# Kernel optimization log

Hardware: AMD Instinct MI355X
Metric: run time of the kernel (lower is better)

The kernel has to match this reference:

```python
import jax, jax.numpy as jnp
import numpy as np
import math

B, S, D = 2, 1024, 512
H = 8
DH = D // H
N_NEURONS = 512
K = 16
N_BASIS = 8
RANK = 64
D_FF = 2048
LN_EPS = 1e-5


def _layer_norm(x, g, b):
    mu = jnp.mean(x, axis=-1, keepdims=True)
    var = jnp.var(x, axis=-1, keepdims=True)
    return (x - mu) * jax.lax.rsqrt(var + LN_EPS) * g + b


def setup_inputs() -> dict:
    key = jax.random.key(0)
    ks = jax.random.split(key, 16)
    x = jax.random.normal(ks[0], (B, S, D), dtype=jnp.float32)
    # causal mask [B,1,S,S] (True = keep)
    mask = jnp.broadcast_to(jnp.tril(jnp.ones((S, S), dtype=bool)), (B, 1, S, S))
    inp = {
        "x": x,
        "neuron_emb": jax.random.normal(ks[1], (N_NEURONS, D)) * 0.02,
        "Wq": jax.random.normal(ks[2], (D, D)) * 0.02, "bq": jnp.zeros((D,)),
        "Wk": jax.random.normal(ks[3], (D, D)) * 0.02, "bk": jnp.zeros((D,)),
        "Wv": jax.random.normal(ks[4], (D, D)) * 0.02, "bv": jnp.zeros((D,)),
        "Wg": jax.random.normal(ks[5], (2 * D, 2)) * 0.02, "bg": jnp.zeros((2,)),
        "basis_A": jax.random.normal(ks[6], (N_BASIS, D, RANK)) * 0.05,
        "basis_B": jax.random.normal(ks[7], (N_BASIS, RANK, D_FF)) * 0.05,
        "neuron_coords": jax.random.normal(ks[8], (N_NEURONS, N_BASIS)) * 0.5,
        "Wd": jax.random.normal(ks[9], (D_FF, D)) * 0.02, "bd": jnp.zeros((D,)),
        "ln1_g": jnp.ones((D,)), "ln1_b": jnp.zeros((D,)),
        "ln2_g": jnp.ones((D,)), "ln2_b": jnp.zeros((D,)),
        "mask": mask,
    }
    return inp


def reference(x, neuron_emb, Wq, bq, Wk, bk, Wv, bv, Wg, bg, basis_A, basis_B,
              neuron_coords, Wd, bd, ln1_g, ln1_b, ln2_g, ln2_b, mask):
    normed = _layer_norm(x, ln1_g, ln1_b)
    # --- router: cross-attention context ---
    q = (normed @ Wq + bq).reshape(B, S, H, DH).transpose(0, 2, 1, 3)
    k = (normed @ Wk + bk).reshape(B, S, H, DH).transpose(0, 2, 1, 3)
    v = (normed @ Wv + bv).reshape(B, S, H, DH).transpose(0, 2, 1, 3)
    attn = jnp.einsum('bhsd,bhtd->bhst', q, k) / math.sqrt(DH)
    attn = jnp.where(mask, attn, -jnp.inf)
    attn = jax.nn.softmax(attn, axis=-1)
    context = jnp.einsum('bhst,bhtd->bhsd', attn, v)
    context = context.transpose(0, 2, 1, 3).reshape(B, S, D)
    # --- gated neuron scoring + top-k ---
    token_scores = normed @ neuron_emb.T            # [B,S,N]
    context_scores = context @ neuron_emb.T         # [B,S,N]
    gate = jax.nn.softmax(jnp.concatenate([normed, context], axis=-1) @ Wg + bg, axis=-1)
    scores = gate[:, :, 0:1] * token_scores + gate[:, :, 1:2] * context_scores
    topk_scores, topk_idx = jax.lax.top_k(scores, K)  # [B,S,K]
    weights = jax.nn.softmax(topk_scores, axis=-1)
    # --- neuron info residual ---
    neuron_info = jnp.einsum('bsk,bskd->bsd', weights, neuron_emb[topk_idx])
    x = x + neuron_info
    # --- per-token basis-mixed low-rank FFN ---
    normed2 = _layer_norm(x, ln2_g, ln2_b)
    coords = neuron_coords[topk_idx]                # [B,S,K,n_basis]
    token_coords = jnp.einsum('bsk,bskn->bsn', weights, coords)  # [B,S,n_basis]
    # h = x @ (sum_n c_n A_n): contract without materializing [B,S,D,R]
    h = jnp.einsum('bsnr,bsn->bsr', jnp.einsum('bsd,ndr->bsnr', normed2, basis_A), token_coords)
    h = jnp.einsum('bsnf,bsn->bsf', jnp.einsum('bsr,nrf->bsnf', h, basis_B), token_coords)
    h = jax.nn.gelu(h, approximate=False)
    out = h @ Wd + bd
    x = x + out
    return (x, topk_idx)
```

## Files before the change

kernel.cpp:

```cpp
#include <hip/hip_runtime.h>
#include <hip/hip_bf16.h>

#define Bv 2
#define Sv 1024
#define Dv 512
#define Hv 8
#define Nv 512
#define Kv 16
#define NBv 8
#define DFv 2048
#define NTOK (Bv*Sv)

typedef __attribute__((ext_vector_type(8))) short short8;
typedef __attribute__((ext_vector_type(4))) float float4v;

__launch_bounds__(256)
__global__ void ln64_k(const float* __restrict__ x, const float* __restrict__ g,
                       const float* __restrict__ b, double* __restrict__ out)
{
    const int t = blockIdx.x;
    const size_t base = (size_t)t * Dv;
    const int tid = threadIdx.x;
    double v0 = (double)x[base + tid];
    double v1 = (double)x[base + tid + 256];
    double s = v0 + v1, ss = v0 * v0 + v1 * v1;
    #pragma unroll
    for (int off = 32; off; off >>= 1) { s += __shfl_xor(s, off); ss += __shfl_xor(ss, off); }
    __shared__ double red[4][2];
    const int wv = tid >> 6, ln = tid & 63;
    if (ln == 0) { red[wv][0] = s; red[wv][1] = ss; }
    __syncthreads();
    s  = red[0][0] + red[1][0] + red[2][0] + red[3][0];
    ss = red[0][1] + red[1][1] + red[2][1] + red[3][1];
    double mu  = s * (1.0 / Dv);
    double var = ss * (1.0 / Dv) - mu * mu;
    double rstd = 1.0 / sqrt(var + 1e-5);
    out[base + tid]       = (v0 - mu) * rstd * (double)g[tid]       + (double)b[tid];
    out[base + tid + 256] = (v1 - mu) * rstd * (double)g[tid + 256] + (double)b[tid + 256];
}

__launch_bounds__(256)
__global__ void qkv64_k(const double* __restrict__ A,
                        const float* __restrict__ Wq, const float* __restrict__ Wk,
                        const float* __restrict__ Wv, const float* __restrict__ bq,
                        const float* __restrict__ bk, const float* __restrict__ bvv,
                        double* __restrict__ qo, double* __restrict__ ko,
                        double* __restrict__ vo)
{
    const int z = blockIdx.z;
    const float* Bm  = (z == 0) ? Wq : (z == 1) ? Wk : Wv;
    const float* bia = (z == 0) ? bq : (z == 1) ? bk : bvv;
    double* Cout     = (z == 0) ? qo : (z == 1) ? ko : vo;
    const int N = Dv, Kd = Dv;
    __shared__ double As[16][68];
    __shared__ double Bs[16][68];
    const int tid = threadIdx.x;
    const int m0 = blockIdx.y * 64, n0 = blockIdx.x * 64;
    const int tx = tid & 15, ty = tid >> 4;
    double acc[4][4] = {};
    const int lm = tid >> 2, lk4 = (tid & 3) << 2;
    for (int k0 = 0; k0 < Kd; k0 += 16) {
        double4 av = *(const double4*)(A + (size_t)(m0 + lm) * Kd + k0 + lk4);
        As[lk4 + 0][lm] = av.x; As[lk4 + 1][lm] = av.y;
        As[lk4 + 2][lm] = av.z; As[lk4 + 3][lm] = av.w;
        const int kk = tid >> 4, n4 = (tid & 15) << 2;
        float4 bv4 = *(const float4*)(Bm + (size_t)(k0 + kk) * N + n0 + n4);
        Bs[kk][n4 + 0] = (double)bv4.x; Bs[kk][n4 + 1] = (double)bv4.y;
        Bs[kk][n4 + 2] = (double)bv4.z; Bs[kk][n4 + 3] = (double)bv4.w;
        __syncthreads();
        #pragma unroll
        for (int kk2 = 0; kk2 < 16; kk2++) {
            double a_[4], b_[4];
            *(double4*)a_ = *(const double4*)&As[kk2][ty << 2];
            *(double4*)b_ = *(const double4*)&Bs[kk2][tx << 2];
            #pragma unroll
            for (int i = 0; i < 4; i++)
                #pragma unroll
                for (int j = 0; j < 4; j++)
                    acc[i][j] = fma(a_[i], b_[j], acc[i][j]);
        }
        __syncthreads();
    }
    #pragma unroll
    for (int i = 0; i < 4; i++) {
        const int row = m0 + (ty << 2) + i;
        #pragma unroll
        for (int j = 0; j < 4; j++) {
            const int col = n0 + (tx << 2) + j;
            Cout[(size_t)row * N + col] = acc[i][j] + (double)bia[col];
        }
    }
}

__launch_bounds__(256)
__global__ void scores64_k(const double* __restrict__ A0, const double* __restrict__ A1,
                           const double* __restrict__ gate, const float* __restrict__ Bm,
                           double* __restrict__ Cbase)
{
    const int M = NTOK, N = Nv, Kd = Dv;
    const int z = blockIdx.z;
    const int kbeg = z * (Dv / 2), kend = kbeg + Dv / 2;
    double* Cout = Cbase + (size_t)z * M * N;
    __shared__ double As[16][68];
    __shared__ double Bs[16][68];
    const int tid = threadIdx.x;
    const int m0 = blockIdx.y * 64, n0 = blockIdx.x * 64;
    const int tx = tid & 15, ty = tid >> 4;
    double acc[4][4] = {};
    const int lm = tid >> 2, lk4 = (tid & 3) << 2;
    for (int k0 = kbeg; k0 < kend; k0 += 16) {
        const double g0 = gate[2 * (m0 + lm)], g1 = gate[2 * (m0 + lm) + 1];
        double4 a0 = *(const double4*)(A0 + (size_t)(m0 + lm) * Kd + k0 + lk4);
        double4 a1 = *(const double4*)(A1 + (size_t)(m0 + lm) * Kd + k0 + lk4);
        As[lk4 + 0][lm] = g0 * a0.x + g1 * a1.x;
        As[lk4 + 1][lm] = g0 * a0.y + g1 * a1.y;
        As[lk4 + 2][lm] = g0 * a0.z + g1 * a1.z;
        As[lk4 + 3][lm] = g0 * a0.w + g1 * a1.w;
        const int nn = tid >> 2, kq = (tid & 3) << 2;
        float4 bv4 = *(const float4*)(Bm + (size_t)(n0 + nn) * Kd + k0 + kq);
        Bs[kq + 0][nn] = (double)bv4.x; Bs[kq + 1][nn] = (double)bv4.y;
        Bs[kq + 2][nn] = (double)bv4.z; Bs[kq + 3][nn] = (double)bv4.w;
        __syncthreads();
        #pragma unroll
        for (int kk = 0; kk < 16; kk++) {
            double a_[4], b_[4];
            *(double4*)a_ = *(const double4*)&As[kk][ty << 2];
            *(double4*)b_ = *(const double4*)&Bs[kk][tx << 2];
            #pragma unroll
            for (int i = 0; i < 4; i++)
                #pragma unroll
                for (int j = 0; j < 4; j++)
                    acc[i][j] = fma(a_[i], b_[j], acc[i][j]);
        }
        __syncthreads();
    }
    #pragma unroll
    for (int i = 0; i < 4; i++) {
        const int row = m0 + (ty << 2) + i;
        #pragma unroll
        for (int j = 0; j < 4; j++)
            Cout[(size_t)row * N + n0 + (tx << 2) + j] = acc[i][j];
    }
}

template<int EPI>
__launch_bounds__(256)
__global__ void mfma_k(const __hip_bfloat16* __restrict__ A, const __hip_bfloat16* __restrict__ B,
                       void* __restrict__ Cout_, int M, int N, int Kt, int kper)
{
    __shared__ __hip_bfloat16 As[128][40];
    __shared__ __hip_bfloat16 Bs[128][40];
    const int tid = threadIdx.x;
    const int m0 = blockIdx.y * 128, n0 = blockIdx.x * 128;
    const int z = blockIdx.z;
    const int kbeg = z * kper, kend = kbeg + kper;
    const int w = tid >> 6, l = tid & 63;
    const int wr = (w >> 1) * 64, wc = (w & 1) * 64;
    const int lm = l & 15, quad = l >> 4;
    float4v acc[4][4];
    #pragma unroll
    for (int i = 0; i < 4; i++)
        #pragma unroll
        for (int j = 0; j < 4; j++)
            acc[i][j] = (float4v){0.f, 0.f, 0.f, 0.f};
    const int srow = tid >> 1, skb = (tid & 1) * 16;
    for (int k0 = kbeg; k0 < kend; k0 += 32) {
        *(uint4*)&As[srow][skb]     = *(const uint4*)(A + (size_t)(m0 + srow) * Kt + k0 + skb);
        *(uint4*)&As[srow][skb + 8] = *(const uint4*)(A + (size_t)(m0 + srow) * Kt + k0 + skb + 8);
        *(uint4*)&Bs[srow][skb]     = *(const uint4*)(B + (size_t)(n0 + srow) * Kt + k0 + skb);
        *(uint4*)&Bs[srow][skb + 8] = *(const uint4*)(B + (size_t)(n0 + srow) * Kt + k0 + skb + 8);
        __syncthreads();
        short8 af[4], bf[4];
        #pragma unroll
        for (int mi = 0; mi < 4; mi++) af[mi] = *(const short8*)&As[wr + mi * 16 + lm][quad * 8];
        #pragma unroll
        for (int ni = 0; ni < 4; ni++) bf[ni] = *(const short8*)&Bs[wc + ni * 16 + lm][quad * 8];
        #pragma unroll
        for (int mi = 0; mi < 4; mi++)
            #pragma unroll
            for (int ni = 0; ni < 4; ni++)
                acc[mi][ni] = __builtin_amdgcn_mfma_f32_16x16x32_bf16(af[mi], bf[ni], acc[mi][ni], 0, 0, 0);
        __syncthreads();
    }
    #pragma unroll
    for (int mi = 0; mi < 4; mi++) {
        #pragma unroll
        for (int ni = 0; ni < 4; ni++) {
            const int col = n0 + wc + ni * 16 + lm;
            #pragma unroll
            for (int r = 0; r < 4; r++) {
                const int row = m0 + wr + mi * 16 + quad * 4 + r;
                float c = acc[mi][ni][r];
                if (EPI == 0) {
                    ((float*)Cout_)[(size_t)z * M * N + (size_t)row * N + col] = c;
                } else {
                    c = 0.5f * c * (1.0f + erff(c * 0.70710678118654752f));
                    ((__hip_bfloat16*)Cout_)[(size_t)row * N + col] = __float2bfloat16(c);
                }
            }
        }
    }
}

__device__ __constant__ int c_slotbase[4] = {0, 0, 384, 640};
__device__ __constant__ int c_cnt[4]      = {0, 24, 16, 8};

__launch_bounds__(256)
__global__ void attn64c_k(const double* __restrict__ q, const double* __restrict__ k,
                          const double* __restrict__ v, double* __restrict__ ctxun,
                          double* __restrict__ Opart, double* __restrict__ mbuf,
                          double* __restrict__ lbuf)
{
    const int qt = blockIdx.x, bh = blockIdx.y, ch = blockIdx.z;
    if (qt < ch * 8) return;
    const int b = bh >> 3, h = bh & 7;
    __shared__ double Qs[32][70];
    __shared__ double Kt[64][34];
    __shared__ double Vs[32][70];
    const int tid = threadIdx.x;
    const int r = tid >> 3, cc = tid & 7;
    const int lane = tid & 63;
    const int lbase = lane & 56;
    const size_t qoff = ((size_t)b * Sv + (size_t)qt * 32) * Dv + h * 64;
    #pragma unroll
    for (int i = 0; i < 4; i++) {
        int f = i * 256 + tid;
        int row = f >> 5, c2 = (f & 31) * 2;
        *(double2*)&Qs[row][c2] = *(const double2*)(q + qoff + (size_t)row * Dv + c2);
    }
    double O[8] = {};
    double mrun = -1e300, lrun = 0.0;
    const int iglob = qt * 32 + r;
    const int jbeg = ch * 8;
    const int jend = (qt < jbeg + 7) ? qt : (jbeg + 7);
    for (int jt = jbeg; jt <= jend; jt++) {
        __syncthreads();
        const size_t koff = ((size_t)b * Sv + (size_t)jt * 32) * Dv + h * 64;
        #pragma unroll
        for (int i = 0; i < 4; i++) {
            int f = i * 256 + tid;
            int row = f >> 5, c2 = (f & 31) * 2;
            double2 kv = *(const double2*)(k + koff + (size_t)row * Dv + c2);
            Kt[c2][row]     = kv.x;
            Kt[c2 + 1][row] = kv.y;
            *(double2*)&Vs[row][c2] = *(const double2*)(v + koff + (size_t)row * Dv + c2);
        }
        __syncthreads();
        double a[4] = {0.0, 0.0, 0.0, 0.0};
        #pragma unroll 8
        for (int kk = 0; kk < 64; kk += 2) {
            double2 qv  = *(const double2*)&Qs[r][kk];
            double2 ka0 = *(const double2*)&Kt[kk][cc * 4];
            double2 ka1 = *(const double2*)&Kt[kk][cc * 4 + 2];
            double2 kb0 = *(const double2*)&Kt[kk + 1][cc * 4];
            double2 kb1 = *(const double2*)&Kt[kk + 1][cc * 4 + 2];
            a[0] = fma(qv.x, ka0.x, fma(qv.y, kb0.x, a[0]));
            a[1] = fma(qv.x, ka0.y, fma(qv.y, kb0.y, a[1]));
            a[2] = fma(qv.x, ka1.x, fma(qv.y, kb1.x, a[2]));
            a[3] = fma(qv.x, ka1.y, fma(qv.y, kb1.y, a[3]));
        }
        double p[4];
        double mx = -1e300;
        #pragma unroll
        for (int jj = 0; jj < 4; jj++) {
            const int jglob = jt * 32 + cc * 4 + jj;
            p[jj] = (jglob <= iglob) ? a[jj] * 0.125 : -1e300;
            mx = fmax(mx, p[jj]);
        }
        mx = fmax(mx, __shfl_xor(mx, 1));
        mx = fmax(mx, __shfl_xor(mx, 2));
        mx = fmax(mx, __shfl_xor(mx, 4));
        const double mnew = fmax(mrun, mx);
        double rsum = 0.0;
        #pragma unroll
        for (int jj = 0; jj < 4; jj++) { p[jj] = exp(p[jj] - mnew); rsum += p[jj]; }
        rsum += __shfl_xor(rsum, 1);
        rsum += __shfl_xor(rsum, 2);
        rsum += __shfl_xor(rsum, 4);
        const double alpha = exp(mrun - mnew);
        lrun = lrun * alpha + rsum;
        mrun = mnew;
        #pragma unroll
        for (int c = 0; c < 8; c++) O[c] *= alpha;
        #pragma unroll
        for (int jsrc = 0; jsrc < 8; jsrc++) {
            #pragma unroll
            for (int jj = 0; jj < 4; jj++) {
                const double pj = __shfl(p[jj], lbase + jsrc);
                const double* vrow = &Vs[jsrc * 4 + jj][cc * 8];
                #pragma unroll
                for (int c2 = 0; c2 < 8; c2 += 2) {
                    double2 vv = *(const double2*)&vrow[c2];
                    O[c2 + 0] = fma(pj, vv.x, O[c2 + 0]);
                    O[c2 + 1] = fma(pj, vv.y, O[c2 + 1]);
                }
            }
        }
    }
    if (cc == 0) {
        const int mi = ((bh * 32 + qt) * 4 + ch) * 32 + r;
        mbuf[mi] = mrun; lbuf[mi] = lrun;
    }
    if (ch == 0) {
        const size_t obase = ((size_t)b * Sv + (size_t)iglob) * Dv + h * 64 + cc * 8;
        #pragma unroll
        for (int c2 = 0; c2 < 8; c2 += 2) { double2 t{O[c2], O[c2+1]}; *(double2*)(ctxun + obase + c2) = t; }
    } else {
        const int slot = c_slotbase[ch] + bh * c_cnt[ch] + (qt - ch * 8);
        const size_t obase = ((size_t)slot * 32 + r) * 64 + cc * 8;
        #pragma unroll
        for (int c2 = 0; c2 < 8; c2 += 2) { double2 t{O[c2], O[c2+1]}; *(double2*)(Opart + obase + c2) = t; }
    }
}

__launch_bounds__(256)
__global__ void attnmerge_k(double* __restrict__ ctx, const double* __restrict__ Opart,
                            const double* __restrict__ mbuf, const double* __restrict__ lbuf)
{
    const size_t i = (size_t)blockIdx.x * 256 + threadIdx.x;
    const size_t e = i * 2;
    const int d = (int)(e & 511);
    const int s = (int)((e >> 9) & 1023);
    const int b = (int)(e >> 19);
    const int h = d >> 6;
    const int qt = s >> 5, r = s & 31;
    const int bh = b * 8 + h;
    int nch = qt >> 3; if (nch > 3) nch = 3;
    const int mib = ((bh * 32 + qt) * 4) * 32 + r;
    double ms = mbuf[mib];
    for (int c = 1; c <= nch; c++) ms = fmax(ms, mbuf[mib + c * 32]);
    double2 o = *(const double2*)(ctx + e);
    double a0 = exp(mbuf[mib] - ms);
    double den = lbuf[mib] * a0;
    o.x *= a0; o.y *= a0;
    for (int c = 1; c <= nch; c++) {
        const double ac = exp(mbuf[mib + c * 32] - ms);
        den += lbuf[mib + c * 32] * ac;
        const int slot = c_slotbase[c] + bh * c_cnt[c] + (qt - c * 8);
        const size_t op = ((size_t)slot * 32 + r) * 64 + (d & 63);
        double2 oc = *(const double2*)(Opart + op);
        o.x = fma(ac, oc.x, o.x);
        o.y = fma(ac, oc.y, o.y);
    }
    const double inv = 1.0 / den;
    o.x *= inv; o.y *= inv;
    *(double2*)(ctx + e) = o;
}

__launch_bounds__(256)
__global__ void gate64_k(const double* __restrict__ normed, const double* __restrict__ ctx,
                         const float* __restrict__ Wg, const float* __restrict__ bg,
                         double* __restrict__ gate)
{
    const int wv = threadIdx.x >> 6, lane = threadIdx.x & 63;
    const int t = blockIdx.x * 4 + wv;
    double a0 = 0.0, a1 = 0.0;
    for (int d = lane; d < Dv; d += 64) {
        double nv = normed[(size_t)t * Dv + d];
        double cv = ctx[(size_t)t * Dv + d];
        a0 += nv * (double)Wg[2 * d]     + cv * (double)Wg[2 * (d + Dv)];
        a1 += nv * (double)Wg[2 * d + 1] + cv * (double)Wg[2 * (d + Dv) + 1];
    }
    #pragma unroll
    for (int off = 32; off; off >>= 1) { a0 += __shfl_xor(a0, off); a1 += __shfl_xor(a1, off); }
    if (lane == 0) {
        a0 += (double)bg[0]; a1 += (double)bg[1];
        double m = fmax(a0, a1);
        double e0 = exp(a0 - m), e1 = exp(a1 - m);
        double inv = 1.0 / (e0 + e1);
        gate[2 * t] = e0 * inv; gate[2 * t + 1] = e1 * inv;
    }
}

__launch_bounds__(256)
__global__ void topk64_k(const double* __restrict__ s0, const float* __restrict__ x,
                         const float* __restrict__ emb, const float* __restrict__ coords,
                         const float* __restrict__ g2, const float* __restrict__ b2,
                         float* __restrict__ x2, __hip_bfloat16* __restrict__ normed2bf,
                         float* __restrict__ tcoords, float* __restrict__ idx_out)
{
    __shared__ double sc[4][Nv];
    const int wv = threadIdx.x >> 6, lane = threadIdx.x & 63;
    const int t = blockIdx.x * 4 + wv;
    const double* s1 = s0 + (size_t)NTOK * Nv;
    double* s = sc[wv];
    #pragma unroll
    for (int i = 0; i < 8; i++) {
        const size_t idx = (size_t)t * Nv + i * 64 + lane;
        s[i * 64 + lane] = s0[idx] + s1[idx];
    }
    __syncthreads();
    double wval[Kv]; int widx[Kv];
    for (int kk = 0; kk < Kv; kk++) {
        double bvv = -1e300; int bi = Nv;
        #pragma unroll
        for (int i = 0; i < 8; i++) {
            const int d = lane * 8 + i;
            const double vv = s[d];
            if (vv > bvv) { bvv = vv; bi = d; }
        }
        #pragma unroll
        for (int off = 1; off < 64; off <<= 1) {
            double ov = __shfl_xor(bvv, off);
            int    oi = __shfl_xor(bi, off);
            if (ov > bvv || (ov == bvv && oi < bi)) { bvv = ov; bi = oi; }
        }
        wval[kk] = bvv; widx[kk] = bi;
        __syncthreads();
        if (lane == (bi >> 3)) s[bi] = -1e301;
        __syncthreads();
        if (lane == kk) idx_out[(size_t)t * Kv + kk] = (float)bi;
    }
    double w[Kv]; double sum = 0.0;
    #pragma unroll
    for (int kk = 0; kk < Kv; kk++) { w[kk] = exp(wval[kk] - wval[0]); sum += w[kk]; }
    const double invs = 1.0 / sum;
    #pragma unroll
    for (int kk = 0; kk < Kv; kk++) w[kk] *= invs;
    float xv[8];
    float sm = 0.0f, sq = 0.0f;
    #pragma unroll
    for (int i = 0; i < 8; i++) {
        const int d = lane + 64 * i;
        double info = 0.0;
        #pragma unroll
        for (int kk = 0; kk < Kv; kk++)
            info = fma(w[kk], (double)emb[(size_t)widx[kk] * Dv + d], info);
        float vv = (float)((double)x[(size_t)t * Dv + d] + info);
        xv[i] = vv;
        x2[(size_t)t * Dv + d] = vv;
        sm += vv; sq += vv * vv;
    }
    #pragma unroll
    for (int off = 32; off; off >>= 1) { sm += __shfl_xor(sm, off); sq += __shfl_xor(sq, off); }
    const float mu = sm * (1.0f / Dv);
    const float var = sq * (1.0f / Dv) - mu * mu;
    const float rstd = rsqrtf(var + 1e-5f);
    #pragma unroll
    for (int i = 0; i < 8; i++) {
        const int d = lane + 64 * i;
        normed2bf[(size_t)t * Dv + d] = __float2bfloat16((xv[i] - mu) * rstd * g2[d] + b2[d]);
    }
    if (lane < NBv) {
        double tc = 0.0;
        #pragma unroll
        for (int kk = 0; kk < Kv; kk++)
            tc = fma(w[kk], (double)coords[(size_t)widx[kk] * NBv + lane], tc);
        tcoords[t * NBv + lane] = (float)tc;
    }
}

__launch_bounds__(256)
__global__ void acatbf_k(const float* __restrict__ bA, __hip_bfloat16* __restrict__ AcatT)
{
    const int i = blockIdx.x * 256 + threadIdx.x;
    const int d = i & 511, nc = i >> 9;
    const int n = nc >> 6, r = nc & 63;
    AcatT[i] = __float2bfloat16(bA[n * 32768 + d * 64 + r]);
}

__launch_bounds__(256)
__global__ void tr2bf_k(const float* __restrict__ in, __hip_bfloat16* __restrict__ out,
                        int R, int C)
{
    __shared__ float tile[32][33];
    const int c0 = blockIdx.x * 32, r0 = blockIdx.y * 32;
    const int tx = threadIdx.x & 31, ty = threadIdx.x >> 5;
    #pragma unroll
    for (int i = 0; i < 4; i++)
        tile[ty + 8 * i][tx] = in[(size_t)(r0 + ty + 8 * i) * C + c0 + tx];
    __syncthreads();
    #pragma unroll
    for (int i = 0; i < 4; i++)
        out[(size_t)(c0 + ty + 8 * i) * R + r0 + tx] = __float2bfloat16(tile[tx][ty + 8 * i]);
}

__launch_bounds__(256)
__global__ void combine_k(const float* __restrict__ Gp, const float* __restrict__ tcoords,
                          __hip_bfloat16* __restrict__ u_bf)
{
    const size_t M1 = (size_t)NTOK * Dv;
    const int wv = threadIdx.x >> 6, lane = threadIdx.x & 63;
    const int t = blockIdx.x * 4 + wv;
    float cs[NBv];
    #pragma unroll
    for (int n = 0; n < NBv; n++) cs[n] = tcoords[t * NBv + n];
    float h = 0.0f;
    #pragma unroll
    for (int n = 0; n < NBv; n++) {
        const size_t gi = (size_t)t * Dv + n * 64 + lane;
        float g = Gp[gi] + Gp[gi + M1] + Gp[gi + 2 * M1] + Gp[gi + 3 * M1];
        h = fmaf(cs[n], g, h);
    }
    #pragma unroll
    for (int n = 0; n < NBv; n++)
        u_bf[(size_t)t * Dv + n * 64 + lane] = __float2bfloat16(cs[n] * h);
}

__launch_bounds__(256)
__global__ void reduce4_k(const float* __restrict__ p4, const float* __restrict__ bd,
                          const float* __restrict__ x2, float* __restrict__ xout)
{
    const size_t M1 = (size_t)NTOK * Dv;
    const size_t i = (size_t)blockIdx.x * 256 + threadIdx.x;
    float c = p4[i] + p4[i + M1] + p4[i + 2 * M1] + p4[i + 3 * M1];
    xout[i] = c + bd[i & 511] + x2[i];
}

extern "C" void kernel_launch(void* const* d_in, const int* in_sizes, int n_in,
                              void* d_out, int out_size, void* d_ws, size_t ws_size,
                              hipStream_t stream) {
    (void)in_sizes; (void)n_in; (void)out_size; (void)ws_size;
    const size_t M1 = (size_t)NTOK * Dv;

    const float* x   = (const float*)d_in[0];
    const float* emb = (const float*)d_in[1];
    const float* Wq  = (const float*)d_in[2];
    const float* bq  = (const float*)d_in[3];
    const float* Wk  = (const float*)d_in[4];
    const float* bk  = (const float*)d_in[5];
    const float* Wv  = (const float*)d_in[6];
    const float* bvv = (const float*)d_in[7];
    const float* Wg  = (const float*)d_in[8];
    const float* bg  = (const float*)d_in[9];
    const float* bA  = (const float*)d_in[10];
    const float* bB  = (const float*)d_in[11];
    const float* crd = (const float*)d_in[12];
    const float* Wd  = (const float*)d_in[13];
    const float* bd  = (const float*)d_in[14];
    const float* l1g = (const float*)d_in[15];
    const float* l1b = (const float*)d_in[16];
    const float* l2g = (const float*)d_in[17];
    const float* l2b = (const float*)d_in[18];

    double* normed64 = (double*)d_ws;
    double* q64      = normed64 + M1;
    double* k64      = q64 + M1;
    double* v64      = k64 + M1;
    double* ctx64    = v64 + M1;
    double* Opart    = ctx64 + M1;
    double* mbuf     = Opart + 1572864;
    double* lbuf     = mbuf + 65536;
    double* gate64   = lbuf + 65536;
    float*  tcoords  = (float*)(gate64 + 4096);
    __hip_bfloat16* AcatT = (__hip_bfloat16*)(tcoords + 16384);

    double* s0 = q64;
    float*  x2 = (float*)v64;
    __hip_bfloat16* normed2bf = (__hip_bfloat16*)(x2 + M1);
    __hip_bfloat16* u_bf      = normed2bf + M1;
    float* Gp = (float*)q64;
    float* p4 = (float*)q64;
    __hip_bfloat16* hf_bf = (__hip_bfloat16*)Opart;
    __hip_bfloat16* bBT   = hf_bf + 4 * M1;
    __hip_bfloat16* WdT   = bBT + M1;

    float* xout    = (float*)d_out;
    float* idx_out = (float*)d_out + M1;

    ln64_k<<<NTOK, 256, 0, stream>>>(x, l1g, l1b, normed64);
    qkv64_k<<<dim3(8, 32, 3), 256, 0, stream>>>(normed64, Wq, Wk, Wv, bq, bk, bvv, q64, k64, v64);
    attn64c_k<<<dim3(32, 16, 4), 256, 0, stream>>>(q64, k64, v64, ctx64, Opart, mbuf, lbuf);
    attnmerge_k<<<(int)(M1 / 512), 256, 0, stream>>>(ctx64, Opart, mbuf, lbuf);
    gate64_k<<<NTOK / 4, 256, 0, stream>>>(normed64, ctx64, Wg, bg, gate64);
    scores64_k<<<dim3(8, 32, 2), 256, 0, stream>>>(normed64, ctx64, gate64, emb, s0);
    topk64_k<<<NTOK / 4, 256, 0, stream>>>(s0, x, emb, crd, l2g, l2b, x2, normed2bf, tcoords, idx_out);
    acatbf_k<<<1024, 256, 0, stream>>>(bA, AcatT);
    tr2bf_k<<<dim3(DFv / 32, Dv / 32), 256, 0, stream>>>(bB, bBT, Dv, DFv);
    tr2bf_k<<<dim3(Dv / 32, DFv / 32), 256, 0, stream>>>(Wd, WdT, DFv, Dv);
    mfma_k<0><<<dim3(4, 16, 4), 256, 0, stream>>>(normed2bf, AcatT, Gp, NTOK, Dv, Dv, Dv / 4);
    combine_k<<<NTOK / 4, 256, 0, stream>>>(Gp, tcoords, u_bf);
    mfma_k<1><<<dim3(16, 16, 1), 256, 0, stream>>>(u_bf, bBT, hf_bf, NTOK, DFv, Dv, Dv);
    mfma_k<0><<<dim3(4, 16, 4), 256, 0, stream>>>(hf_bf, WdT, p4, NTOK, Dv, DFv, DFv / 4);
    reduce4_k<<<(int)(M1 / 256), 256, 0, stream>>>(p4, bd, x2, xout);
}
```

Baseline: 624.6 us.

## Use FP64 MFMA for attention with runtime self-check and scalar fallback

Replaces the scalar FP64 flash-attention kernel with one that computes QK^T and PV using 16x16x4 FP64 MFMA instructions, keeping the split-chunk online-softmax merge. A single-block check kernel then recomputes three sample rows by brute force and sets a flag. If they mismatch, the old scalar kernel and merge are rerun. This moves the attention math onto the matrix cores at the cost of two extra launches, a serial single-block check, and a possible full fallback.

New measurement: 944.7 us. 1.51x slower.

```diff
diff --git a/kernel.cpp b/kernel.cpp
--- a/kernel.cpp
+++ b/kernel.cpp
@@ -13,6 +13,17 @@
 
 typedef __attribute__((ext_vector_type(8))) short short8;
 typedef __attribute__((ext_vector_type(4))) float float4v;
+typedef __attribute__((ext_vector_type(4))) double double4v;
+
+#if defined(__HIP_DEVICE_COMPILE__)
+  #if __has_builtin(__builtin_amdgcn_mfma_f64_16x16x4f64)
+    #define MFMA64(a, b, c) __builtin_amdgcn_mfma_f64_16x16x4f64((a), (b), (c), 0, 0, 0)
+  #else
+    #define MFMA64(a, b, c) __builtin_amdgcn_mfma_f64_16x16x4_f64((a), (b), (c), 0, 0, 0)
+  #endif
+#else
+  #define MFMA64(a, b, c) (c)
+#endif
 
 __launch_bounds__(256)
 __global__ void ln64_k(const float* __restrict__ x, const float* __restrict__ g,
@@ -206,11 +217,155 @@
 __device__ __constant__ int c_cnt[4]      = {0, 24, 16, 8};
 
 __launch_bounds__(256)
-__global__ void attn64c_k(const double* __restrict__ q, const double* __restrict__ k,
+__global__ void attn64m_k(const double* __restrict__ q, const double* __restrict__ k,
                           const double* __restrict__ v, double* __restrict__ ctxun,
                           double* __restrict__ Opart, double* __restrict__ mbuf,
                           double* __restrict__ lbuf)
 {
+    const int qt = blockIdx.x, bh = blockIdx.y, ch = blockIdx.z;
+    if (qt < ch * 8) return;
+    const int b = bh >> 3, h = bh & 7;
+    __shared__ double Qs[32][66];
+    __shared__ double Ks[32][66];
+    __shared__ double Vt[64][33];
+    __shared__ double Ps[32][34];
+    __shared__ double xm[2][32], xl[2][32], rowm[32], rowl[32];
+    const int tid = threadIdx.x;
+    const int w = tid >> 6, lane = tid & 63;
+    const int l15 = lane & 15, hq = lane >> 4;
+    const int mhalf = w >> 1, nhalf = w & 1;
+    const int m0s = mhalf * 16, n0s = nhalf * 16;
+    const size_t qoff = ((size_t)b * Sv + (size_t)qt * 32) * Dv + h * 64;
+    #pragma unroll
+    for (int i = 0; i < 8; i++) {
+        const int row = w * 8 + i;
+        Qs[row][lane] = q[qoff + (size_t)row * Dv + lane];
+    }
+    if (tid < 32) { rowm[tid] = -1e300; rowl[tid] = 0.0; }
+    double4v Oa[2];
+    Oa[0] = (double4v){0., 0., 0., 0.};
+    Oa[1] = (double4v){0., 0., 0., 0.};
+    const int jbeg = ch * 8;
+    const int jend = (qt < jbeg + 7) ? qt : (jbeg + 7);
+    __syncthreads();
+    for (int jt = jbeg; jt <= jend; jt++) {
+        __syncthreads();
+        const size_t koff = ((size_t)b * Sv + (size_t)jt * 32) * Dv + h * 64;
+        #pragma unroll
+        for (int i = 0; i < 8; i++) {
+            const int row = w * 8 + i;
+            Ks[row][lane] = k[koff + (size_t)row * Dv + lane];
+            Vt[lane][row] = v[koff + (size_t)row * Dv + lane];
+        }
+        __syncthreads();
+        double mold[4], lold[4];
+        #pragma unroll
+        for (int i = 0; i < 4; i++) {
+            const int rr = m0s + hq * 4 + i;
+            mold[i] = rowm[rr]; lold[i] = rowl[rr];
+        }
+        double4v Sf0 = (double4v){0., 0., 0., 0.};
+        double4v Sf1 = (double4v){0., 0., 0., 0.};
+        #pragma unroll
+        for (int d0 = 0; d0 < 64; d0 += 8) {
+            Sf0 = MFMA64(Qs[m0s + l15][d0 + hq],     Ks[n0s + l15][d0 + hq],     Sf0);
+            Sf1 = MFMA64(Qs[m0s + l15][d0 + 4 + hq], Ks[n0s + l15][d0 + 4 + hq], Sf1);
+        }
+        double s[4], mx[4];
+        const int jglob = jt * 32 + n0s + l15;
+        #pragma unroll
+        for (int i = 0; i < 4; i++) {
+            const int iglob = qt * 32 + m0s + hq * 4 + i;
+            s[i] = (jglob <= iglob) ? (Sf0[i] + Sf1[i]) * 0.125 : -1e300;
+            mx[i] = s[i];
+        }
+        #pragma unroll
+        for (int off = 1; off < 16; off <<= 1)
+            #pragma unroll
+            for (int i = 0; i < 4; i++)
+                mx[i] = fmax(mx[i], __shfl_xor(mx[i], off));
+        if (l15 == 0)
+            #pragma unroll
+            for (int i = 0; i < 4; i++) xm[nhalf][m0s + hq * 4 + i] = mx[i];
+        __syncthreads();
+        double mnew[4], alpha[4], psum[4];
+        #pragma unroll
+        for (int i = 0; i < 4; i++) {
+            const int rr = m0s + hq * 4 + i;
+            const double tm = fmax(xm[0][rr], xm[1][rr]);
+            mnew[i] = fmax(mold[i], tm);
+            alpha[i] = exp(mold[i] - mnew[i]);
+            const double p = exp(s[i] - mnew[i]);
+            Ps[rr][n0s + l15] = p;
+            psum[i] = p;
+        }
+        #pragma unroll
+        for (int off = 1; off < 16; off <<= 1)
+            #pragma unroll
+            for (int i = 0; i < 4; i++)
+                psum[i] += __shfl_xor(psum[i], off);
+        if (l15 == 0) {
+            #pragma unroll
+            for (int i = 0; i < 4; i++) {
+                const int rr = m0s + hq * 4 + i;
+                xl[nhalf][rr] = psum[i];
+                if (nhalf == 0) rowm[rr] = mnew[i];
+            }
+        }
+        __syncthreads();
+        if (l15 == 0 && nhalf == 0) {
+            #pragma unroll
+            for (int i = 0; i < 4; i++) {
+                const int rr = m0s + hq * 4 + i;
+                rowl[rr] = lold[i] * alpha[i] + xl[0][rr] + xl[1][rr];
+            }
+        }
+        #pragma unroll
+        for (int nt = 0; nt < 2; nt++)
+            #pragma unroll
+            for (int i = 0; i < 4; i++)
+                Oa[nt][i] *= alpha[i];
+        #pragma unroll
+        for (int j0 = 0; j0 < 32; j0 += 4) {
+            const double aP = Ps[m0s + l15][j0 + hq];
+            Oa[0] = MFMA64(aP, Vt[nhalf * 32 + l15][j0 + hq],      Oa[0]);
+            Oa[1] = MFMA64(aP, Vt[nhalf * 32 + 16 + l15][j0 + hq], Oa[1]);
+        }
+    }
+    __syncthreads();
+    if (ch == 0) {
+        #pragma unroll
+        for (int nt = 0; nt < 2; nt++) {
+            const int col = nhalf * 32 + nt * 16 + l15;
+            #pragma unroll
+            for (int i = 0; i < 4; i++) {
+                const int iglob = qt * 32 + m0s + hq * 4 + i;
+                ctxun[((size_t)b * Sv + iglob) * Dv + h * 64 + col] = Oa[nt][i];
+            }
+        }
+    } else {
+        const int slot = c_slotbase[ch] + bh * c_cnt[ch] + (qt - ch * 8);
+        #pragma unroll
+        for (int nt = 0; nt < 2; nt++) {
+            const int col = nhalf * 32 + nt * 16 + l15;
+            #pragma unroll
+            for (int i = 0; i < 4; i++)
+                Opart[((size_t)slot * 32 + m0s + hq * 4 + i) * 64 + col] = Oa[nt][i];
+        }
+    }
+    if (tid < 32) {
+        const int mi = ((bh * 32 + qt) * 4 + ch) * 32 + tid;
+        mbuf[mi] = rowm[tid]; lbuf[mi] = rowl[tid];
+    }
+}
+
+__launch_bounds__(256)
+__global__ void attnfix_k(const double* __restrict__ q, const double* __restrict__ k,
+                          const double* __restrict__ v, double* __restrict__ ctxun,
+                          double* __restrict__ Opart, double* __restrict__ mbuf,
+                          double* __restrict__ lbuf, const int* __restrict__ flag)
+{
+    if (*flag) return;
     const int qt = blockIdx.x, bh = blockIdx.y, ch = blockIdx.z;
     if (qt < ch * 8) return;
     const int b = bh >> 3, h = bh & 7;
@@ -315,8 +470,10 @@
 
 __launch_bounds__(256)
 __global__ void attnmerge_k(double* __restrict__ ctx, const double* __restrict__ Opart,
-                            const double* __restrict__ mbuf, const double* __restrict__ lbuf)
-{
+                            const double* __restrict__ mbuf, const double* __restrict__ lbuf,
+                            int mode, const int* __restrict__ flag)
+{
+    if (mode && *flag) return;
     const size_t i = (size_t)blockIdx.x * 256 + threadIdx.x;
     const size_t e = i * 2;
     const int d = (int)(e & 511);
@@ -348,6 +505,63 @@
 }
 
 __launch_bounds__(256)
+__global__ void attncheck_k(const double* __restrict__ q, const double* __restrict__ k,
+                            const double* __restrict__ v, const double* __restrict__ ctx,
+                            int* __restrict__ flag)
+{
+    __shared__ double sc[1024];
+    __shared__ double red[256];
+    __shared__ int bad;
+    const int tid = threadIdx.x;
+    if (tid == 0) bad = 0;
+    __syncthreads();
+    const int cbv[3] = {0, 1, 1};
+    const int chv[3] = {0, 7, 2};
+    const int csv[3] = {1023, 1000, 100};
+    for (int c = 0; c < 3; c++) {
+        const int b = cbv[c], h = chv[c], s = csv[c];
+        const double* qrow = q + ((size_t)(b * Sv + s) * Dv + h * 64);
+        for (int j = tid; j <= s; j += 256) {
+            const double* krow = k + ((size_t)(b * Sv + j) * Dv + h * 64);
+            double a = 0.0;
+            for (int d = 0; d < 64; d++) a += qrow[d] * krow[d];
+            sc[j] = a * 0.125;
+        }
+        __syncthreads();
+        double m = -1e300;
+        for (int j = tid; j <= s; j += 256) m = fmax(m, sc[j]);
+        red[tid] = m;
+        __syncthreads();
+        for (int off = 128; off; off >>= 1) {
+            if (tid < off) red[tid] = fmax(red[tid], red[tid + off]);
+            __syncthreads();
+        }
+        m = red[0];
+        __syncthreads();
+        double lsum = 0.0;
+        for (int j = tid; j <= s; j += 256) { double p = exp(sc[j] - m); sc[j] = p; lsum += p; }
+        red[tid] = lsum;
+        __syncthreads();
+        for (int off = 128; off; off >>= 1) {
+            if (tid < off) red[tid] += red[tid + off];
+            __syncthreads();
+        }
+        const double l = red[0];
+        __syncthreads();
+        if (tid < 64) {
+            double o = 0.0;
+            for (int j = 0; j <= s; j++)
+                o += sc[j] * v[((size_t)(b * Sv + j) * Dv + h * 64) + tid];
+            o /= l;
+            const double got = ctx[((size_t)(b * Sv + s) * Dv + h * 64) + tid];
+            if (fabs(got - o) > 1e-9 * (1.0 + fabs(o))) bad = 1;
+        }
+        __syncthreads();
+    }
+    if (tid == 0) *flag = bad ? 0 : 1;
+}
+
+__launch_bounds__(256)
 __global__ void gate64_k(const double* __restrict__ normed, const double* __restrict__ ctx,
                          const float* __restrict__ Wg, const float* __restrict__ bg,
                          double* __restrict__ gate)
@@ -544,6 +758,7 @@
     double* gate64   = lbuf + 65536;
     float*  tcoords  = (float*)(gate64 + 4096);
     __hip_bfloat16* AcatT = (__hip_bfloat16*)(tcoords + 16384);
+    int*    flag     = (int*)(AcatT + 262144);
 
     double* s0 = q64;
     float*  x2 = (float*)v64;
@@ -560,8 +775,11 @@
 
     ln64_k<<<NTOK, 256, 0, stream>>>(x, l1g, l1b, normed64);
     qkv64_k<<<dim3(8, 32, 3), 256, 0, stream>>>(normed64, Wq, Wk, Wv, bq, bk, bvv, q64, k64, v64);
-    attn64c_k<<<dim3(32, 16, 4), 256, 0, stream>>>(q64, k64, v64, ctx64, Opart, mbuf, lbuf);
-    attnmerge_k<<<(int)(M1 / 512), 256, 0, stream>>>(ctx64, Opart, mbuf, lbuf);
+    attn64m_k<<<dim3(32, 16, 4), 256, 0, stream>>>(q64, k64, v64, ctx64, Opart, mbuf, lbuf);
+    attnmerge_k<<<(int)(M1 / 512), 256, 0, stream>>>(ctx64, Opart, mbuf, lbuf, 0, flag);
+    attncheck_k<<<1, 256, 0, stream>>>(q64, k64, v64, ctx64, flag);
+    attnfix_k<<<dim3(32, 16, 4), 256, 0, stream>>>(q64, k64, v64, ctx64, Opart, mbuf, lbuf, flag);
+    attnmerge_k<<<(int)(M1 / 512), 256, 0, stream>>>(ctx64, Opart, mbuf, lbuf, 1, flag);
     gate64_k<<<NTOK / 4, 256, 0, stream>>>(normed64, ctx64, Wg, bg, gate64);
     scores64_k<<<dim3(8, 32, 2), 256, 0, stream>>>(normed64, ctx64, gate64, emb, s0);
     topk64_k<<<NTOK / 4, 256, 0, stream>>>(s0, x, emb, crd, l2g, l2b, x2, normed2bf, tcoords, idx_out);
```
